# Optimization experiments

Measured on AMD Instinct MI355X. Metric: run time of the kernel, lower is better.

## Reference

```python
import jax, jax.numpy as jnp
import numpy as np

B, S, H, NH = 4, 2048, 1024, 16
HS = H // NH


def setup_inputs() -> dict:
    key = jax.random.key(0)
    ks = jax.random.split(key, 9)
    s = 0.02
    return {
        "x": jax.random.normal(ks[0], (B, S, H), dtype=jnp.float32),
        "Wq": jax.random.normal(ks[1], (H, H), dtype=jnp.float32) * s,
        "bq": jnp.zeros((H,), dtype=jnp.float32),
        "Wk": jax.random.normal(ks[2], (H, H), dtype=jnp.float32) * s,
        "bk": jnp.zeros((H,), dtype=jnp.float32),
        "Wv": jax.random.normal(ks[3], (H, H), dtype=jnp.float32) * s,
        "bv": jnp.zeros((H,), dtype=jnp.float32),
        "Wp": jax.random.normal(ks[4], (H, H), dtype=jnp.float32) * s,
        "bp": jnp.zeros((H,), dtype=jnp.float32),
    }


def _split_heads(t):
    # [B,S,H] -> [B,NH,S,HS]
    b, s, _ = t.shape
    return t.reshape(b, s, NH, HS).swapaxes(1, 2)


def reference(x, Wq, bq, Wk, bk, Wv, bv, Wp, bp):
    # torch Linear: y = x @ W.T + b
    q = _split_heads(x @ Wq.T + bq)
    k = _split_heads(x @ Wk.T + bk)
    v = _split_heads(x @ Wv.T + bv)
    scale = 1.0 / np.sqrt(HS).astype(np.float32)
    scores = jnp.einsum('bhqd,bhkd->bhqk', q, k) * scale  # [B,NH,S,S]
    n_pos = scores.shape[2]
    causal = jnp.arange(n_pos)[None, :] <= jnp.arange(n_pos)[:, None]
    mask_value = jnp.finfo(scores.dtype).min
    scores = jnp.where(causal, scores, mask_value)
    attn_w = jax.nn.softmax(scores, axis=-1)
    # dropout is identity in eval mode
    attn = jnp.einsum('bhqk,bhkd->bhqd', attn_w, v)
    attn = attn.swapaxes(1, 2).reshape(x.shape[0], n_pos, H)
    return attn @ Wp.T + bp
```

## Files before the change

kernel.cpp:

```cpp
#include <hip/hip_runtime.h>

#define B_ 4
#define S_ 2048
#define H_ 1024
#define NH_ 16
#define HS_ 64
#define SG_ (B_*S_)

typedef __bf16 bf16x8 __attribute__((ext_vector_type(8)));
typedef __bf16 bf16x4 __attribute__((ext_vector_type(4)));
typedef float  f32x4  __attribute__((ext_vector_type(4)));

__device__ __forceinline__ void gload16(const void* g, void* l) {
    __builtin_amdgcn_global_load_lds(
        (const __attribute__((address_space(1))) void*)g,
        (__attribute__((address_space(3))) void*)l,
        16, 0, 0);
}

__global__ void cvt_f32_bf16(const float* __restrict__ in, __bf16* __restrict__ out, int n4) {
    int i = blockIdx.x * blockDim.x + threadIdx.x;
    if (i >= n4) return;
    float4 v = reinterpret_cast<const float4*>(in)[i];
    bf16x4 o;
    o[0] = (__bf16)v.x; o[1] = (__bf16)v.y; o[2] = (__bf16)v.z; o[3] = (__bf16)v.w;
    reinterpret_cast<bf16x4*>(out)[i] = o;
}

__global__ void cvt_w4(const float* __restrict__ w0, const float* __restrict__ w1,
                       const float* __restrict__ w2, const float* __restrict__ w3,
                       __bf16* __restrict__ o0, __bf16* __restrict__ o1,
                       __bf16* __restrict__ o2, __bf16* __restrict__ o3, int n4) {
    int i = blockIdx.x * blockDim.x + threadIdx.x;
    if (i >= n4) return;
    const float* in; __bf16* out;
    switch (blockIdx.y) {
        case 0: in = w0; out = o0; break;
        case 1: in = w1; out = o1; break;
        case 2: in = w2; out = o2; break;
        default: in = w3; out = o3; break;
    }
    float4 v = reinterpret_cast<const float4*>(in)[i];
    bf16x4 o;
    o[0] = (__bf16)v.x; o[1] = (__bf16)v.y; o[2] = (__bf16)v.z; o[3] = (__bf16)v.w;
    reinterpret_cast<bf16x4*>(out)[i] = o;
}

__device__ __forceinline__ void store_tile(const f32x4& acc, long mbase, long nbase, int lane,
                                           const float* __restrict__ bias, void* __restrict__ out,
                                           long N, int out_f32, int bias_row) {
    const int r16 = lane & 15, kg = lane >> 4;
    const long col = nbase + r16;
    const float bc = bias_row ? 0.f : bias[col];
#pragma unroll
    for (int r = 0; r < 4; ++r) {
        const long row = mbase + kg * 4 + r;
        const float v = acc[r] + (bias_row ? bias[row] : bc);
        if (out_f32) ((float*)out)[row * N + col] = v;
        else         ((__bf16*)out)[row * N + col] = (__bf16)v;
    }
}

__global__ __launch_bounds__(256) void gemm128(
    const __bf16* __restrict__ A, const __bf16* __restrict__ W,
    const float* __restrict__ bias, void* __restrict__ out,
    int M, int N, int K, int out_f32, int bias_row)
{
    __shared__ __bf16 sA[128][64];
    __shared__ __bf16 sB[128][64];
    const int lane = threadIdx.x & 63, widx = threadIdx.x >> 6;
    const int wr = widx >> 1, wc = widx & 1;
    const int c = lane & 15, g = lane >> 4;
    const long m0 = (long)blockIdx.y * 128, n0 = (long)blockIdx.x * 128;
    const int sr8 = lane >> 3;
    const int sc8 = lane & 7;

    f32x4 acc[4][4] = {};

    for (int k0 = 0; k0 < K; k0 += 64) {
#pragma unroll
        for (int it = 0; it < 4; ++it) {
            const int rb = it * 32 + widx * 8;
            const int row = rb + sr8;
            gload16(A + (m0 + row) * K + k0 + ((sc8 ^ (row & 7)) << 3), &sA[rb][0]);
            gload16(W + (n0 + row) * K + k0 + ((sc8 ^ (row & 7)) << 3), &sB[rb][0]);
        }
        __syncthreads();
        bf16x8 af[2][4], bfr[2][4];
#pragma unroll
        for (int i = 0; i < 4; ++i) {
            const int ra = wr * 64 + i * 16 + c;
            const char* ap = (const char*)&sA[ra][0];
            af[0][i] = *(const bf16x8*)(ap + ((( g    ) ^ (ra & 7)) << 4));
            af[1][i] = *(const bf16x8*)(ap + (((4 | g) ^ (ra & 7)) << 4));
            const int rbn = wc * 64 + i * 16 + c;
            const char* bp = (const char*)&sB[rbn][0];
            bfr[0][i] = *(const bf16x8*)(bp + ((( g    ) ^ (rbn & 7)) << 4));
            bfr[1][i] = *(const bf16x8*)(bp + (((4 | g) ^ (rbn & 7)) << 4));
        }
#pragma unroll
        for (int kh = 0; kh < 2; ++kh)
#pragma unroll
            for (int i = 0; i < 4; ++i)
#pragma unroll
                for (int j = 0; j < 4; ++j)
                    acc[i][j] = __builtin_amdgcn_mfma_f32_16x16x32_bf16(af[kh][i], bfr[kh][j], acc[i][j], 0, 0, 0);
        __syncthreads();
    }

#pragma unroll
    for (int i = 0; i < 4; ++i)
#pragma unroll
        for (int j = 0; j < 4; ++j)
            store_tile(acc[i][j], m0 + wr * 64 + i * 16, n0 + wc * 64 + j * 16,
                       lane, bias, out, N, out_f32, bias_row);
}

__global__ __launch_bounds__(256) void attn_mfma2(
    const __bf16* __restrict__ Q, const __bf16* __restrict__ Kg,
    const __bf16* __restrict__ Vt, __bf16* __restrict__ Ab)
{
    __shared__ __bf16 ldsK[64][64];
    __shared__ __bf16 ldsV[64][64];
    __shared__ __bf16 ldsE[4][32 * 72];

    const int lane = threadIdx.x & 63, widx = threadIdx.x >> 6;
    const int c = lane & 15, g = lane >> 4;
    const int bid = blockIdx.x;
    const int bh = bid & 63, pi = bid >> 6;
    const int b = bh >> 4, h = bh & 15;

    const int sr8 = lane >> 3;
    const int sc8 = lane & 7;
    const float qscale = 0.125f * 1.4426950408889634f;

    for (int seg = 0; seg < 2; ++seg) {
        const int chunk = seg ? (15 - pi) : pi;
        const int q0w = chunk * 128 + widx * 32;

        bf16x8 qf[2][2];
#pragma unroll
        for (int qi = 0; qi < 2; ++qi)
#pragma unroll
            for (int hf = 0; hf < 2; ++hf) {
                const long qa = ((long)(b * S_ + q0w + qi * 16 + c)) * H_ + h * HS_ + hf * 32 + g * 8;
                bf16x8 t = *reinterpret_cast<const bf16x8*>(Q + qa);
#pragma unroll
                for (int j = 0; j < 8; ++j) t[j] = (__bf16)(qscale * (float)t[j]);
                qf[qi][hf] = t;
            }

        f32x4 ot[4][2] = {};
        float m[2] = {-1e30f, -1e30f}, l[2] = {0.f, 0.f};
        const int nt = 2 * (chunk + 1);

        for (int t = 0; t < nt; ++t) {
            const int kt = t * 64;
#pragma unroll
            for (int it = 0; it < 2; ++it) {
                const int row = widx * 16 + it * 8 + sr8;
                gload16(Kg + ((long)(b * S_ + kt + row)) * H_ + h * HS_ + ((sc8 ^ (row & 7)) << 3),
                        &ldsK[widx * 16 + it * 8][0]);
            }
#pragma unroll
            for (int it = 0; it < 2; ++it) {
                const int dr = widx * 16 + it * 8 + sr8;
                gload16(Vt + ((long)(h * HS_ + dr)) * SG_ + b * S_ + kt + ((sc8 ^ (dr & 7)) << 3),
                        &ldsV[widx * 16 + it * 8][0]);
            }
            __syncthreads();

            if (kt <= q0w + 31) {
                f32x4 st[4][2] = {};
#pragma unroll
                for (int t4 = 0; t4 < 4; ++t4) {
                    const int r = t4 * 16 + c;
                    const char* kp = (const char*)&ldsK[r][0];
                    bf16x8 kf0 = *(const bf16x8*)(kp + (((g)     ^ (c & 7)) << 4));
                    bf16x8 kf1 = *(const bf16x8*)(kp + (((4 | g) ^ (c & 7)) << 4));
#pragma unroll
                    for (int qi = 0; qi < 2; ++qi) {
                        st[t4][qi] = __builtin_amdgcn_mfma_f32_16x16x32_bf16(kf0, qf[qi][0], st[t4][qi], 0, 0, 0);
                        st[t4][qi] = __builtin_amdgcn_mfma_f32_16x16x32_bf16(kf1, qf[qi][1], st[t4][qi], 0, 0, 0);
                    }
                }
                if (kt + 63 > q0w) {
#pragma unroll
                    for (int t4 = 0; t4 < 4; ++t4)
#pragma unroll
                        for (int qi = 0; qi < 2; ++qi)
#pragma unroll
                            for (int r = 0; r < 4; ++r)
                                if (kt + t4 * 16 + g * 4 + r > q0w + qi * 16 + c)
                                    st[t4][qi][r] = -1e30f;
                }
                bf16x8 pf[2][2];
                float fr[2];
#pragma unroll
                for (int qi = 0; qi < 2; ++qi) {
                    float pm = -1e30f;
#pragma unroll
                    for (int t4 = 0; t4 < 4; ++t4)
#pragma unroll
                        for (int r = 0; r < 4; ++r) pm = fmaxf(pm, st[t4][qi][r]);
                    pm = fmaxf(pm, __shfl_xor(pm, 16));
                    pm = fmaxf(pm, __shfl_xor(pm, 32));
                    const float mn = fmaxf(m[qi], pm);
                    fr[qi] = exp2f(m[qi] - mn);
                    m[qi] = mn;
                    float p[16], rs = 0.f;
#pragma unroll
                    for (int t4 = 0; t4 < 4; ++t4)
#pragma unroll
                        for (int r = 0; r < 4; ++r) {
                            const float e = exp2f(st[t4][qi][r] - mn);
                            p[t4 * 4 + r] = e; rs += e;
                        }
                    rs += __shfl_xor(rs, 16);
                    rs += __shfl_xor(rs, 32);
                    l[qi] = l[qi] * fr[qi] + rs;
#pragma unroll
                    for (int j = 0; j < 8; ++j) {
                        pf[0][qi][j] = (__bf16)p[j];
                        pf[1][qi][j] = (__bf16)p[8 + j];
                    }
                }
#pragma unroll
                for (int blk = 0; blk < 4; ++blk) {
#pragma unroll
                    for (int qi = 0; qi < 2; ++qi) ot[blk][qi] *= fr[qi];
                    const char* vp = (const char*)&ldsV[blk * 16 + c][0];
                    const int sw = c & 7;
#pragma unroll
                    for (int hf = 0; hf < 2; ++hf) {
                        bf16x4 lo = *(const bf16x4*)(vp + ((((hf << 2) + (g >> 1))     ^ sw) << 4) + ((g & 1) << 3));
                        bf16x4 hi = *(const bf16x4*)(vp + ((((hf << 2) + 2 + (g >> 1)) ^ sw) << 4) + ((g & 1) << 3));
                        bf16x8 vf;
                        vf[0] = lo[0]; vf[1] = lo[1]; vf[2] = lo[2]; vf[3] = lo[3];
                        vf[4] = hi[0]; vf[5] = hi[1]; vf[6] = hi[2]; vf[7] = hi[3];
#pragma unroll
                        for (int qi = 0; qi < 2; ++qi)
                            ot[blk][qi] = __builtin_amdgcn_mfma_f32_16x16x32_bf16(vf, pf[hf][qi], ot[blk][qi], 0, 0, 0);
                    }
                }
            }
            __syncthreads();
        }

        __bf16* myo = ldsE[widx];
#pragma unroll
        for (int qi = 0; qi < 2; ++qi) {
            const float invl = 1.0f / l[qi];
#pragma unroll
            for (int blk = 0; blk < 4; ++blk) {
                bf16x4 tv;
#pragma unroll
                for (int r = 0; r < 4; ++r) tv[r] = (__bf16)(ot[blk][qi][r] * invl);
                *reinterpret_cast<bf16x4*>(myo + (qi * 16 + c) * 72 + blk * 16 + g * 4) = tv;
            }
        }
#pragma unroll
        for (int half = 0; half < 2; ++half) {
            const int qr = lane >> 2, dc = (lane & 3) * 16;
            const __bf16* src = myo + (half * 16 + qr) * 72 + dc;
            bf16x8 r0 = *reinterpret_cast<const bf16x8*>(src);
            bf16x8 r1 = *reinterpret_cast<const bf16x8*>(src + 8);
            __bf16* dst = Ab + ((long)(b * S_ + q0w + half * 16 + qr)) * H_ + h * HS_ + dc;
            *reinterpret_cast<bf16x8*>(dst) = r0;
            *reinterpret_cast<bf16x8*>(dst + 8) = r1;
        }
    }
}

extern "C" void kernel_launch(void* const* d_in, const int* in_sizes, int n_in,
                              void* d_out, int out_size, void* d_ws, size_t ws_size,
                              hipStream_t stream) {
    const float* x  = (const float*)d_in[0];
    const float* Wq = (const float*)d_in[1];
    const float* bq = (const float*)d_in[2];
    const float* Wk = (const float*)d_in[3];
    const float* bk = (const float*)d_in[4];
    const float* Wv = (const float*)d_in[5];
    const float* bv = (const float*)d_in[6];
    const float* Wp = (const float*)d_in[7];
    const float* bp = (const float*)d_in[8];
    float* out = (float*)d_out;

    const int M = SG_;
    const int N = H_;
    const int K = H_;

    char* ws = (char*)d_ws;
    size_t off = 0;
    __bf16* xb  = (__bf16*)(ws + off); off += (size_t)M * K * 2;
    __bf16* Wqb = (__bf16*)(ws + off); off += (size_t)N * K * 2;
    __bf16* Wkb = (__bf16*)(ws + off); off += (size_t)N * K * 2;
    __bf16* Wvb = (__bf16*)(ws + off); off += (size_t)N * K * 2;
    __bf16* Wpb = (__bf16*)(ws + off); off += (size_t)N * K * 2;
    __bf16* Qb  = (__bf16*)(ws + off); off += (size_t)M * H_ * 2;
    __bf16* Kbf = (__bf16*)(ws + off); off += (size_t)M * H_ * 2;
    __bf16* Vt  = (__bf16*)(ws + off); off += (size_t)M * H_ * 2;
    __bf16* Ab  = (__bf16*)(ws + off); off += (size_t)M * H_ * 2;

    {
        int n4 = M * K / 4;
        cvt_f32_bf16<<<(n4 + 255) / 256, 256, 0, stream>>>(x, xb, n4);
        int w4 = N * K / 4;
        dim3 gw((w4 + 255) / 256, 4);
        cvt_w4<<<gw, 256, 0, stream>>>(Wq, Wk, Wv, Wp, Wqb, Wkb, Wvb, Wpb, w4);
    }

    dim3 gg(N / 128, M / 128);
    gemm128<<<gg, 256, 0, stream>>>(xb, Wqb, bq, Qb,  M, N, K, 0, 0);
    gemm128<<<gg, 256, 0, stream>>>(xb, Wkb, bk, Kbf, M, N, K, 0, 0);
    dim3 gv(M / 128, N / 128);
    gemm128<<<gv, 256, 0, stream>>>(Wvb, xb, bv, Vt, N, M, K, 0, 1);

    attn_mfma2<<<512, 256, 0, stream>>>(Qb, Kbf, Vt, Ab);

    gemm128<<<gg, 256, 0, stream>>>(Ab, Wpb, bp, out, M, N, K, 1, 0);
}
```

Baseline: 314.6 us.

## Double-buffer LDS tiles in GEMM and attention; defer softmax rescaling

Both the projection GEMM and the attention kernel now keep two LDS buffers. The next K-tile (or next K/V tile) is issued with global_load_lds before the current tile is computed, so global loads overlap the MFMA work. This drops one barrier per iteration, at the cost of doubling LDS use, which may reduce occupancy. The attention softmax also uses a flatter 3-input max reduction, and it skips updating the running max and rescaling the output accumulator when every lane's new max is within 8 (log2 units) of the old one.

```diff
diff --git a/kernel.cpp b/kernel.cpp
--- a/kernel.cpp
+++ b/kernel.cpp
@@ -10,6 +10,8 @@
 typedef __bf16 bf16x8 __attribute__((ext_vector_type(8)));
 typedef __bf16 bf16x4 __attribute__((ext_vector_type(4)));
 typedef float  f32x4  __attribute__((ext_vector_type(4)));
+
+#define M3(a,b,c) fmaxf(fmaxf((a),(b)),(c))
 
 __device__ __forceinline__ void gload16(const void* g, void* l) {
     __builtin_amdgcn_global_load_lds(
@@ -66,8 +68,8 @@
     const float* __restrict__ bias, void* __restrict__ out,
     int M, int N, int K, int out_f32, int bias_row)
 {
-    __shared__ __bf16 sA[128][64];
-    __shared__ __bf16 sB[128][64];
+    __shared__ __bf16 sA[2][128][64];
+    __shared__ __bf16 sB[2][128][64];
     const int lane = threadIdx.x & 63, widx = threadIdx.x >> 6;
     const int wr = widx >> 1, wc = widx & 1;
     const int c = lane & 15, g = lane >> 4;
@@ -75,26 +77,34 @@
     const int sr8 = lane >> 3;
     const int sc8 = lane & 7;
 
-    f32x4 acc[4][4] = {};
-
-    for (int k0 = 0; k0 < K; k0 += 64) {
+    auto STAGE = [&](int buf, int k0) {
 #pragma unroll
         for (int it = 0; it < 4; ++it) {
             const int rb = it * 32 + widx * 8;
             const int row = rb + sr8;
-            gload16(A + (m0 + row) * K + k0 + ((sc8 ^ (row & 7)) << 3), &sA[rb][0]);
-            gload16(W + (n0 + row) * K + k0 + ((sc8 ^ (row & 7)) << 3), &sB[rb][0]);
-        }
-        __syncthreads();
+            gload16(A + (m0 + row) * K + k0 + ((sc8 ^ (row & 7)) << 3), &sA[buf][rb][0]);
+            gload16(W + (n0 + row) * K + k0 + ((sc8 ^ (row & 7)) << 3), &sB[buf][rb][0]);
+        }
+    };
+
+    f32x4 acc[4][4] = {};
+
+    STAGE(0, 0);
+    __syncthreads();
+    const int NK = K >> 6;
+    for (int kt = 0; kt < NK; ++kt) {
+        const int cur = kt & 1;
+        if (kt + 1 < NK) STAGE(cur ^ 1, (kt + 1) << 6);
+
         bf16x8 af[2][4], bfr[2][4];
 #pragma unroll
         for (int i = 0; i < 4; ++i) {
             const int ra = wr * 64 + i * 16 + c;
-            const char* ap = (const char*)&sA[ra][0];
+            const char* ap = (const char*)&sA[cur][ra][0];
             af[0][i] = *(const bf16x8*)(ap + ((( g    ) ^ (ra & 7)) << 4));
             af[1][i] = *(const bf16x8*)(ap + (((4 | g) ^ (ra & 7)) << 4));
             const int rbn = wc * 64 + i * 16 + c;
-            const char* bp = (const char*)&sB[rbn][0];
+            const char* bp = (const char*)&sB[cur][rbn][0];
             bfr[0][i] = *(const bf16x8*)(bp + ((( g    ) ^ (rbn & 7)) << 4));
             bfr[1][i] = *(const bf16x8*)(bp + (((4 | g) ^ (rbn & 7)) << 4));
         }
@@ -120,8 +130,8 @@
     const __bf16* __restrict__ Q, const __bf16* __restrict__ Kg,
     const __bf16* __restrict__ Vt, __bf16* __restrict__ Ab)
 {
-    __shared__ __bf16 ldsK[64][64];
-    __shared__ __bf16 ldsV[64][64];
+    __shared__ __bf16 ldsK[2][64][64];
+    __shared__ __bf16 ldsV[2][64][64];
     __shared__ __bf16 ldsE[4][32 * 72];
 
     const int lane = threadIdx.x & 63, widx = threadIdx.x >> 6;
@@ -134,6 +144,21 @@
     const int sc8 = lane & 7;
     const float qscale = 0.125f * 1.4426950408889634f;
 
+    auto STAGEKV = [&](int buf, int kt) {
+#pragma unroll
+        for (int it = 0; it < 2; ++it) {
+            const int row = widx * 16 + it * 8 + sr8;
+            gload16(Kg + ((long)(b * S_ + kt + row)) * H_ + h * HS_ + ((sc8 ^ (row & 7)) << 3),
+                    &ldsK[buf][widx * 16 + it * 8][0]);
+        }
+#pragma unroll
+        for (int it = 0; it < 2; ++it) {
+            const int dr = widx * 16 + it * 8 + sr8;
+            gload16(Vt + ((long)(h * HS_ + dr)) * SG_ + b * S_ + kt + ((sc8 ^ (dr & 7)) << 3),
+                    &ldsV[buf][widx * 16 + it * 8][0]);
+        }
+    };
+
     for (int seg = 0; seg < 2; ++seg) {
         const int chunk = seg ? (15 - pi) : pi;
         const int q0w = chunk * 128 + widx * 32;
@@ -154,28 +179,20 @@
         float m[2] = {-1e30f, -1e30f}, l[2] = {0.f, 0.f};
         const int nt = 2 * (chunk + 1);
 
+        STAGEKV(0, 0);
+        __syncthreads();
+
         for (int t = 0; t < nt; ++t) {
+            const int cur = t & 1;
+            if (t + 1 < nt) STAGEKV(cur ^ 1, (t + 1) * 64);
             const int kt = t * 64;
-#pragma unroll
-            for (int it = 0; it < 2; ++it) {
-                const int row = widx * 16 + it * 8 + sr8;
-                gload16(Kg + ((long)(b * S_ + kt + row)) * H_ + h * HS_ + ((sc8 ^ (row & 7)) << 3),
-                        &ldsK[widx * 16 + it * 8][0]);
-            }
-#pragma unroll
-            for (int it = 0; it < 2; ++it) {
-                const int dr = widx * 16 + it * 8 + sr8;
-                gload16(Vt + ((long)(h * HS_ + dr)) * SG_ + b * S_ + kt + ((sc8 ^ (dr & 7)) << 3),
-                        &ldsV[widx * 16 + it * 8][0]);
-            }
-            __syncthreads();
 
             if (kt <= q0w + 31) {
                 f32x4 st[4][2] = {};
 #pragma unroll
                 for (int t4 = 0; t4 < 4; ++t4) {
                     const int r = t4 * 16 + c;
-                    const char* kp = (const char*)&ldsK[r][0];
+                    const char* kp = (const char*)&ldsK[cur][r][0];
                     bf16x8 kf0 = *(const bf16x8*)(kp + (((g)     ^ (c & 7)) << 4));
                     bf16x8 kf1 = *(const bf16x8*)(kp + (((4 | g) ^ (c & 7)) << 4));
 #pragma unroll
@@ -196,18 +213,27 @@
                 }
                 bf16x8 pf[2][2];
                 float fr[2];
+                int resc = 0;
 #pragma unroll
                 for (int qi = 0; qi < 2; ++qi) {
-                    float pm = -1e30f;
-#pragma unroll
-                    for (int t4 = 0; t4 < 4; ++t4)
-#pragma unroll
-                        for (int r = 0; r < 4; ++r) pm = fmaxf(pm, st[t4][qi][r]);
+                    const float a0 = M3(st[0][qi][0], st[0][qi][1], st[0][qi][2]);
+                    const float a1 = M3(st[0][qi][3], st[1][qi][0], st[1][qi][1]);
+                    const float a2 = M3(st[1][qi][2], st[1][qi][3], st[2][qi][0]);
+                    const float a3 = M3(st[2][qi][1], st[2][qi][2], st[2][qi][3]);
+                    const float a4 = M3(st[3][qi][0], st[3][qi][1], st[3][qi][2]);
+                    float pm = M3(M3(a0, a1, a2), a3, fmaxf(a4, st[3][qi][3]));
                     pm = fmaxf(pm, __shfl_xor(pm, 16));
                     pm = fmaxf(pm, __shfl_xor(pm, 32));
-                    const float mn = fmaxf(m[qi], pm);
-                    fr[qi] = exp2f(m[qi] - mn);
-                    m[qi] = mn;
+                    const int defer = __all(pm - m[qi] <= 8.0f);
+                    float mn;
+                    if (defer) {
+                        mn = m[qi]; fr[qi] = 1.0f;
+                    } else {
+                        mn = fmaxf(m[qi], pm);
+                        fr[qi] = exp2f(m[qi] - mn);
+                        m[qi] = mn;
+                        resc = 1;
+                    }
                     float p[16], rs = 0.f;
 #pragma unroll
                     for (int t4 = 0; t4 < 4; ++t4)
@@ -225,11 +251,16 @@
                         pf[1][qi][j] = (__bf16)p[8 + j];
                     }
                 }
+                if (resc) {
+#pragma unroll
+                    for (int blk = 0; blk < 4; ++blk) {
+                        ot[blk][0] *= fr[0];
+                        ot[blk][1] *= fr[1];
+                    }
+                }
 #pragma unroll
                 for (int blk = 0; blk < 4; ++blk) {
-#pragma unroll
-                    for (int qi = 0; qi < 2; ++qi) ot[blk][qi] *= fr[qi];
-                    const char* vp = (const char*)&ldsV[blk * 16 + c][0];
+                    const char* vp = (const char*)&ldsV[cur][blk * 16 + c][0];
                     const int sw = c & 7;
 #pragma unroll
                     for (int hf = 0; hf < 2; ++hf) {
```

Result: faster. 306.9 us (-2.4%).
